# Kernel optimization log

Measured on AMD Instinct MI355X. Metric: run time of the kernel, lower is better.

Reference implementation:

```python
import jax, jax.numpy as jnp
import numpy as np

B, H, OUT, C, O = 4096, 32, 16, 16, 80
N = C + O          # node_num
T = 5              # time_step


def setup_inputs() -> dict:
    key = jax.random.key(0)
    ks = jax.random.split(key, 24)
    x = jax.random.normal(ks[0], (B, N * H), jnp.float32)
    # relation matrix [num_classes, num_objects] -> block adjacency as in load_nodes
    mat = (jax.random.uniform(ks[1], (C, O)) < 0.3).astype(jnp.float32)
    in_mat = jnp.zeros((N, N), jnp.float32).at[:C, C:].set(mat)
    out_mat = jnp.zeros((N, N), jnp.float32).at[C:, :C].set(mat.T)
    mask = (mat > 0).astype(jnp.float32)  # [C, O]

    def W(k, o, i, s=0.1):
        return (jax.random.normal(k, (o, i), jnp.float32) * s)

    return dict(
        input=x, in_mat=in_mat, out_mat=out_mat, mask=mask,
        W3w=W(ks[2], H, 2 * H), b3w=jnp.zeros((H,), jnp.float32),
        W3u=W(ks[3], H, H),     b3u=jnp.zeros((H,), jnp.float32),
        W4w=W(ks[4], H, 2 * H), b4w=jnp.zeros((H,), jnp.float32),
        W5w=W(ks[5], H, 2 * H), b5w=jnp.zeros((H,), jnp.float32),
        W5u=W(ks[6], H, H),     b5u=jnp.zeros((H,), jnp.float32),
        Wo=W(ks[7], OUT, 2 * H), bo=jnp.zeros((OUT,), jnp.float32),
        Wrx=W(ks[8], OUT, H, 0.01), brx=jnp.zeros((OUT,), jnp.float32),
        Wry=W(ks[9], OUT, H, 0.01), bry=jnp.zeros((OUT,), jnp.float32),
        Wr2=W(ks[10], 1, OUT, 0.1), br2=jnp.zeros((1,), jnp.float32),
    )


def reference(input, in_mat, out_mat, mask, W3w, b3w, W3u, b3u, W4w, b4w,
              W5w, b5w, W5u, b5u, Wo, bo, Wrx, brx, Wry, bry, Wr2, br2):
    x0 = input.reshape(B, N, H)
    nodes = x0
    for _ in range(T):
        a_in = jnp.einsum('ij,bjh->bih', in_mat, nodes)
        a_out = jnp.einsum('ij,bjh->bih', out_mat, nodes)
        av = jnp.concatenate([a_in, a_out], axis=-1)          # [B,N,2H]
        u3 = nodes @ W3u.T + b3u
        zv = jax.nn.sigmoid(av @ W3w.T + b3w + u3)
        # NOTE: original code (bug) reuses fc_eq3_u for the reset gate
        rv = jax.nn.sigmoid(av @ W4w.T + b4w + u3)
        hv = jnp.tanh(av @ W5w.T + b5w + (rv * nodes) @ W5u.T + b5u)
        nodes = (1.0 - zv) * nodes + zv * hv
    # per-node output
    out = jnp.tanh(jnp.concatenate([nodes, x0], axis=-1) @ Wo.T + bo)  # [B,N,OUT]
    # pairwise reasoning between class nodes and object nodes
    rfcx = jnp.tanh(nodes[:, :C] @ Wrx.T + brx)   # [B,C,OUT]
    rfcy = jnp.tanh(nodes[:, C:] @ Wry.T + bry)   # [B,O,OUT]
    rocat = rfcx[:, :, None, :] * rfcy[:, None, :, :]              # [B,C,O,OUT]
    rfc2 = jax.nn.sigmoid(rocat @ Wr2.T + br2)                     # [B,C,O,1]
    rfc2 = rfc2 * mask[None, :, :, None]
    routput = out[:, :C]                                           # [B,C,OUT]
    ooutput = out[:, C:]                                           # [B,O,OUT]
    weight_o = ooutput[:, None, :, :] * rfc2                       # [B,C,O,OUT]
    final = jnp.concatenate([routput[:, :, None, :], weight_o], axis=2)  # [B,C,O+1,OUT]
    return final
```

## Files before the change

### kernel.cpp

```cpp
#include <hip/hip_runtime.h>

#define NTH 256

#define S_NDS   0
#define S_AV    3264
#define S_W3U   6528
#define S_W5U   7552
#define S_W3W   8576
#define S_W4W   10624
#define S_W5W   12672
#define S_MASK  14720
#define S_TOT   16016

#define S_WOT   S_W3U
#define S_WRX   S_W5U
#define S_WRY   (S_W5U+512)
#define S_OUTB  S_W3W
#define S_RFCX  S_W4W
#define S_RFCY  (S_W4W+256)
#define S_RFC2  S_AV

__device__ __forceinline__ float sig_(float x) { return 1.0f / (1.0f + __expf(-x)); }
__device__ __forceinline__ float th_(float x)  { return 1.0f - 2.0f / (1.0f + __expf(2.0f * x)); }

union F4 { float4 v; float f[4]; };
union F2 { float2 v; float f[2]; };

__global__ __launch_bounds__(NTH, 2)
void ggnn_fused(const float* __restrict__ input,
                const float* __restrict__ maskp,
                const float* __restrict__ W3w, const float* __restrict__ b3w,
                const float* __restrict__ W3u, const float* __restrict__ b3u,
                const float* __restrict__ W4w, const float* __restrict__ b4w,
                const float* __restrict__ W5w, const float* __restrict__ b5w,
                const float* __restrict__ W5u, const float* __restrict__ b5u,
                const float* __restrict__ Wo,  const float* __restrict__ bo,
                const float* __restrict__ Wrx, const float* __restrict__ brx,
                const float* __restrict__ Wry, const float* __restrict__ bry,
                const float* __restrict__ Wr2, const float* __restrict__ br2,
                float* __restrict__ dout)
{
    __shared__ float S[S_TOT];
    const int tid = threadIdx.x;
    const int b   = blockIdx.x;

    for (int t = tid; t < 1024; t += NTH) {
        const int h = t >> 5, k = t & 31;
        S[S_W3U + k*32 + h] = W3u[t];
        S[S_W5U + k*32 + h] = W5u[t];
    }
    for (int t = tid; t < 2048; t += NTH) {
        const int h = t >> 6, k = t & 63;
        S[S_W3W + k*32 + h] = W3w[t];
        S[S_W4W + k*32 + h] = W4w[t];
        S[S_W5W + k*32 + h] = W5w[t];
    }
    for (int t = tid; t < 1280; t += NTH) {
        const int c = t / 80, o = t - c*80;
        S[S_MASK + c*81 + o] = maskp[t];
    }
    const float* xin = input + (size_t)b * 3072;
    for (int t = tid; t < 3072; t += NTH) {
        const int i = t >> 5, h = t & 31;
        S[S_NDS + i*34 + h] = xin[t];
    }

    const int a  = tid & 31;
    const int bq = tid >> 5;
    const int h0 = bq << 2;
    const int i0 = a, i1 = a + 32, i2 = a + 64;
    const bool isC = (a < 16);

    float bu_[4], bz_[4], br_[4], bh_[4];
    #pragma unroll
    for (int q = 0; q < 4; ++q) {
        bu_[q] = b3u[h0+q];
        bz_[q] = b3w[h0+q];
        br_[q] = b4w[h0+q];
        bh_[q] = b5w[h0+q] + b5u[h0+q];
    }
    __syncthreads();

    for (int it = 0; it < 5; ++it) {
        {
            float a0 = 0.f, a1 = 0.f;
            #pragma unroll 8
            for (int o = 0; o < 80; ++o) {
                const float v = S[S_NDS + (16+o)*34 + a];
                a0 = fmaf(S[S_MASK + bq*81 + o],     v, a0);
                a1 = fmaf(S[S_MASK + (bq+8)*81 + o], v, a1);
            }
            S[S_AV + bq*34 + a]     = a0;
            S[S_AV + (bq+8)*34 + a] = a1;

            float vc[16];
            #pragma unroll
            for (int c = 0; c < 16; ++c) vc[c] = S[S_NDS + c*34 + a];
            #pragma unroll
            for (int tp = 0; tp < 10; ++tp) {
                const int o0 = bq + 8*tp;
                float acc = 0.f;
                #pragma unroll
                for (int c = 0; c < 16; ++c)
                    acc = fmaf(S[S_MASK + c*81 + o0], vc[c], acc);
                S[S_AV + (16+o0)*34 + a] = acc;
            }
        }
        __syncthreads();

        float u0[4],u1[4],u2[4],z0[4],z1[4],z2[4],r0[4],r1[4],r2[4],g0[4],g1[4],g2[4];
        #pragma unroll
        for (int q = 0; q < 4; ++q) {
            u0[q]=bu_[q]; u1[q]=bu_[q]; u2[q]=bu_[q];
            z0[q]=bz_[q]; z1[q]=bz_[q]; z2[q]=bz_[q];
            r0[q]=br_[q]; r1[q]=br_[q]; r2[q]=br_[q];
            g0[q]=bh_[q]; g1[q]=bh_[q]; g2[q]=bh_[q];
        }
        #pragma unroll 2
        for (int k = 0; k < 32; ++k) {
            const float vn0 = S[S_NDS + i0*34 + k];
            const float vn1 = S[S_NDS + i1*34 + k];
            const float vn2 = S[S_NDS + i2*34 + k];
            const float va0 = S[S_AV + i0*34 + k];
            const float va1 = S[S_AV + i1*34 + k];
            const float va2 = S[S_AV + i2*34 + k];
            F4 wu, wzC, wzO, wrC, wrO, whC, whO;
            wu.v  = *(const float4*)&S[S_W3U + k*32 + h0];
            wzC.v = *(const float4*)&S[S_W3W + k*32 + h0];
            wzO.v = *(const float4*)&S[S_W3W + (k+32)*32 + h0];
            wrC.v = *(const float4*)&S[S_W4W + k*32 + h0];
            wrO.v = *(const float4*)&S[S_W4W + (k+32)*32 + h0];
            whC.v = *(const float4*)&S[S_W5W + k*32 + h0];
            whO.v = *(const float4*)&S[S_W5W + (k+32)*32 + h0];
            #pragma unroll
            for (int q = 0; q < 4; ++q) {
                const float wuq = wu.f[q];
                u0[q] = fmaf(wuq, vn0, u0[q]);
                u1[q] = fmaf(wuq, vn1, u1[q]);
                u2[q] = fmaf(wuq, vn2, u2[q]);
                const float wz0 = isC ? wzC.f[q] : wzO.f[q];
                const float wr0 = isC ? wrC.f[q] : wrO.f[q];
                const float wh0 = isC ? whC.f[q] : whO.f[q];
                z0[q] = fmaf(wz0,      va0, z0[q]);
                z1[q] = fmaf(wzO.f[q], va1, z1[q]);
                z2[q] = fmaf(wzO.f[q], va2, z2[q]);
                r0[q] = fmaf(wr0,      va0, r0[q]);
                r1[q] = fmaf(wrO.f[q], va1, r1[q]);
                r2[q] = fmaf(wrO.f[q], va2, r2[q]);
                g0[q] = fmaf(wh0,      va0, g0[q]);
                g1[q] = fmaf(whO.f[q], va1, g1[q]);
                g2[q] = fmaf(whO.f[q], va2, g2[q]);
            }
        }
        float nd0[4], nd1[4], nd2[4];
        #pragma unroll
        for (int q = 0; q < 4; ++q) {
            nd0[q] = S[S_NDS + i0*34 + h0 + q];
            nd1[q] = S[S_NDS + i1*34 + h0 + q];
            nd2[q] = S[S_NDS + i2*34 + h0 + q];
        }
        __syncthreads();
        #pragma unroll
        for (int q = 0; q < 4; ++q) {
            S[S_AV + i0*34 + h0 + q] = sig_(r0[q] + u0[q]) * nd0[q];
            S[S_AV + i1*34 + h0 + q] = sig_(r1[q] + u1[q]) * nd1[q];
            S[S_AV + i2*34 + h0 + q] = sig_(r2[q] + u2[q]) * nd2[q];
        }
        __syncthreads();
        #pragma unroll 4
        for (int k = 0; k < 32; ++k) {
            const float rk0 = S[S_AV + i0*34 + k];
            const float rk1 = S[S_AV + i1*34 + k];
            const float rk2 = S[S_AV + i2*34 + k];
            F4 w5; w5.v = *(const float4*)&S[S_W5U + k*32 + h0];
            #pragma unroll
            for (int q = 0; q < 4; ++q) {
                g0[q] = fmaf(w5.f[q], rk0, g0[q]);
                g1[q] = fmaf(w5.f[q], rk1, g1[q]);
                g2[q] = fmaf(w5.f[q], rk2, g2[q]);
            }
        }
        #pragma unroll
        for (int q = 0; q < 4; ++q) {
            const float zz0 = sig_(z0[q] + u0[q]);
            const float zz1 = sig_(z1[q] + u1[q]);
            const float zz2 = sig_(z2[q] + u2[q]);
            S[S_NDS + i0*34 + h0 + q] = fmaf(zz0, th_(g0[q]) - nd0[q], nd0[q]);
            S[S_NDS + i1*34 + h0 + q] = fmaf(zz1, th_(g1[q]) - nd1[q], nd1[q]);
            S[S_NDS + i2*34 + h0 + q] = fmaf(zz2, th_(g2[q]) - nd2[q], nd2[q]);
        }
        __syncthreads();
    }

    for (int t = tid; t < 3072; t += NTH) {
        const int i = t >> 5, h = t & 31;
        S[S_AV + i*34 + h] = xin[t];
    }
    for (int t = tid; t < 1024; t += NTH) {
        const int j = t >> 6, k = t & 63;
        S[S_WOT + k*16 + j] = Wo[t];
    }
    for (int t = tid; t < 512; t += NTH) {
        const int j = t >> 5, k = t & 31;
        S[S_WRX + k*16 + j] = Wrx[t];
        S[S_WRY + k*16 + j] = Wry[t];
    }
    __syncthreads();

    {
        const int j2 = bq * 2;
        float oa0[2], oa1[2], oa2[2];
        #pragma unroll
        for (int q = 0; q < 2; ++q) { oa0[q] = bo[j2+q]; oa1[q] = bo[j2+q]; oa2[q] = bo[j2+q]; }
        #pragma unroll 2
        for (int k = 0; k < 32; ++k) {
            const float vn0 = S[S_NDS + i0*34 + k];
            const float vn1 = S[S_NDS + i1*34 + k];
            const float vn2 = S[S_NDS + i2*34 + k];
            const float vx0 = S[S_AV + i0*34 + k];
            const float vx1 = S[S_AV + i1*34 + k];
            const float vx2 = S[S_AV + i2*34 + k];
            F2 wn, wx;
            wn.v = *(const float2*)&S[S_WOT + k*16 + j2];
            wx.v = *(const float2*)&S[S_WOT + (32+k)*16 + j2];
            #pragma unroll
            for (int q = 0; q < 2; ++q) {
                oa0[q] = fmaf(wn.f[q], vn0, oa0[q]); oa0[q] = fmaf(wx.f[q], vx0, oa0[q]);
                oa1[q] = fmaf(wn.f[q], vn1, oa1[q]); oa1[q] = fmaf(wx.f[q], vx1, oa1[q]);
                oa2[q] = fmaf(wn.f[q], vn2, oa2[q]); oa2[q] = fmaf(wx.f[q], vx2, oa2[q]);
            }
        }
        #pragma unroll
        for (int q = 0; q < 2; ++q) {
            S[S_OUTB + i0*20 + j2 + q] = th_(oa0[q]);
            S[S_OUTB + i1*20 + j2 + q] = th_(oa1[q]);
            S[S_OUTB + i2*20 + j2 + q] = th_(oa2[q]);
        }
    }
    {
        const int jj = tid & 15, grp = tid >> 4;
        float ax = brx[jj];
        #pragma unroll 4
        for (int k = 0; k < 32; ++k)
            ax = fmaf(S[S_WRX + k*16 + jj], S[S_NDS + grp*34 + k], ax);
        S[S_RFCX + grp*16 + jj] = th_(ax);

        float ay[5];
        #pragma unroll
        for (int t2 = 0; t2 < 5; ++t2) ay[t2] = bry[jj];
        #pragma unroll 2
        for (int k = 0; k < 32; ++k) {
            const float w = S[S_WRY + k*16 + jj];
            #pragma unroll
            for (int t2 = 0; t2 < 5; ++t2)
                ay[t2] = fmaf(w, S[S_NDS + (16 + grp + 16*t2)*34 + k], ay[t2]);
        }
        #pragma unroll
        for (int t2 = 0; t2 < 5; ++t2)
            S[S_RFCY + (grp + 16*t2)*16 + jj] = th_(ay[t2]);
    }
    __syncthreads();

    {
        float wr2r[16];
        #pragma unroll
        for (int j = 0; j < 16; ++j) wr2r[j] = Wr2[j];
        const float br2v = br2[0];
        #pragma unroll
        for (int t2 = 0; t2 < 5; ++t2) {
            const int idx = tid + NTH*t2;
            const int c = idx / 80;
            const int o = idx - c*80;
            float s = br2v;
            #pragma unroll
            for (int j = 0; j < 16; ++j)
                s = fmaf(wr2r[j], S[S_RFCX + c*16 + j] * S[S_RFCY + o*16 + j], s);
            S[S_RFC2 + idx] = sig_(s) * S[S_MASK + c*81 + o];
        }
    }
    __syncthreads();

    {
        float* doutb = dout + (size_t)b * 20736;
        #pragma unroll
        for (int t2 = 0; t2 < 21; ++t2) {
            const int f4 = tid + NTH*t2;
            if (f4 < 5184) {
                const int f   = f4 << 2;
                const int c   = f / 1296;
                const int rem = f - c*1296;
                const int co  = rem >> 4;
                const int k   = rem & 15;
                float4 v;
                if (co == 0) {
                    v = *(const float4*)&S[S_OUTB + c*20 + k];
                } else {
                    const float sc = S[S_RFC2 + c*80 + (co - 1)];
                    const float4 ov = *(const float4*)&S[S_OUTB + (16 + co - 1)*20 + k];
                    v.x = ov.x*sc; v.y = ov.y*sc; v.z = ov.z*sc; v.w = ov.w*sc;
                }
                *(float4*)&doutb[f] = v;
            }
        }
    }
}

extern "C" void kernel_launch(void* const* d_in, const int* in_sizes, int n_in,
                              void* d_out, int out_size, void* d_ws, size_t ws_size,
                              hipStream_t stream) {
    const float* input = (const float*)d_in[0];
    const float* maskp = (const float*)d_in[3];
    const float* W3w = (const float*)d_in[4];  const float* b3w = (const float*)d_in[5];
    const float* W3u = (const float*)d_in[6];  const float* b3u = (const float*)d_in[7];
    const float* W4w = (const float*)d_in[8];  const float* b4w = (const float*)d_in[9];
    const float* W5w = (const float*)d_in[10]; const float* b5w = (const float*)d_in[11];
    const float* W5u = (const float*)d_in[12]; const float* b5u = (const float*)d_in[13];
    const float* Wo  = (const float*)d_in[14]; const float* bo  = (const float*)d_in[15];
    const float* Wrx = (const float*)d_in[16]; const float* brx = (const float*)d_in[17];
    const float* Wry = (const float*)d_in[18]; const float* bry = (const float*)d_in[19];
    const float* Wr2 = (const float*)d_in[20]; const float* br2 = (const float*)d_in[21];

    ggnn_fused<<<dim3(4096), dim3(NTH), 0, stream>>>(
        input, maskp, W3w, b3w, W3u, b3u, W4w, b4w, W5w, b5w, W5u, b5u,
        Wo, bo, Wrx, brx, Wry, bry, Wr2, br2, (float*)d_out);
}
```

Measured before the change: 1.005 ms.

## Move weights to global workspace, shrink LDS, use mask bitmasks and packed FMA

Adds a one-block prep kernel that transposes the weights, folds the biases and packs the adjacency mask into bitmasks in a workspace buffer. The main kernel then reads weights from global memory and cache instead of staging them in LDS. That cuts LDS per block from about 64KB to about 25KB and raises launch bounds to 4 blocks per CU. The adjacency aggregation now uses bitmask selects instead of float mask multiplies, and the GRU matmuls use 2-wide float vectors so the compiler can emit packed FMA. The risk is that weight reads go through the cache instead of LDS, and that register pressure under the tighter launch bound may cause spills.

```diff
diff --git a/kernel.cpp b/kernel.cpp
--- a/kernel.cpp
+++ b/kernel.cpp
@@ -1,264 +1,284 @@
 #include <hip/hip_runtime.h>
 
 #define NTH 256
-
-#define S_NDS   0
-#define S_AV    3264
-#define S_W3U   6528
-#define S_W5U   7552
-#define S_W3W   8576
-#define S_W4W   10624
-#define S_W5W   12672
-#define S_MASK  14720
-#define S_TOT   16016
-
-#define S_WOT   S_W3U
-#define S_WRX   S_W5U
-#define S_WRY   (S_W5U+512)
-#define S_OUTB  S_W3W
-#define S_RFCX  S_W4W
-#define S_RFCY  (S_W4W+256)
-#define S_RFC2  S_AV
+typedef __attribute__((ext_vector_type(2))) float f32x2;
+
+#define WS_WU    0
+#define WS_W5U   1024
+#define WS_WZ    2048
+#define WS_WR    4096
+#define WS_WG    6144
+#define WS_WO    8192
+#define WS_WRX   9216
+#define WS_WRY   9728
+#define WS_BZ    10240
+#define WS_BR    10272
+#define WS_BG    10304
+#define WS_BITC  10336
+#define WS_BITO  10400
+#define WS_TOTAL 10480
 
 __device__ __forceinline__ float sig_(float x) { return 1.0f / (1.0f + __expf(-x)); }
 __device__ __forceinline__ float th_(float x)  { return 1.0f - 2.0f / (1.0f + __expf(2.0f * x)); }
-
-union F4 { float4 v; float f[4]; };
-union F2 { float2 v; float f[2]; };
-
-__global__ __launch_bounds__(NTH, 2)
-void ggnn_fused(const float* __restrict__ input,
-                const float* __restrict__ maskp,
-                const float* __restrict__ W3w, const float* __restrict__ b3w,
-                const float* __restrict__ W3u, const float* __restrict__ b3u,
-                const float* __restrict__ W4w, const float* __restrict__ b4w,
-                const float* __restrict__ W5w, const float* __restrict__ b5w,
-                const float* __restrict__ W5u, const float* __restrict__ b5u,
-                const float* __restrict__ Wo,  const float* __restrict__ bo,
-                const float* __restrict__ Wrx, const float* __restrict__ brx,
-                const float* __restrict__ Wry, const float* __restrict__ bry,
-                const float* __restrict__ Wr2, const float* __restrict__ br2,
-                float* __restrict__ dout)
+__device__ __forceinline__ f32x2 sp(float x) { f32x2 r; r[0] = x; r[1] = x; return r; }
+__device__ __forceinline__ float msel(float v, unsigned bits, int bit) {
+    const int m = (int)(bits << (31 - bit)) >> 31;
+    return __int_as_float(__float_as_int(v) & m);
+}
+
+__global__ void ggnn_prep(const float* __restrict__ mask,
+                          const float* __restrict__ W3w, const float* __restrict__ b3w,
+                          const float* __restrict__ W3u, const float* __restrict__ b3u,
+                          const float* __restrict__ W4w, const float* __restrict__ b4w,
+                          const float* __restrict__ W5w, const float* __restrict__ b5w,
+                          const float* __restrict__ W5u, const float* __restrict__ b5u,
+                          const float* __restrict__ Wo,
+                          const float* __restrict__ Wrx, const float* __restrict__ Wry,
+                          float* __restrict__ ws)
 {
-    __shared__ float S[S_TOT];
+    const int t = threadIdx.x;
+    for (int i = t; i < 1024; i += NTH) {
+        const int k = i >> 5, h = i & 31;
+        ws[WS_WU  + i] = W3u[h*32 + k];
+        ws[WS_W5U + i] = W5u[h*32 + k];
+        ws[WS_WZ + i]        = W3w[h*64 + k];
+        ws[WS_WZ + 1024 + i] = W3w[h*64 + 32 + k];
+        ws[WS_WR + i]        = W4w[h*64 + k];
+        ws[WS_WR + 1024 + i] = W4w[h*64 + 32 + k];
+        ws[WS_WG + i]        = W5w[h*64 + k];
+        ws[WS_WG + 1024 + i] = W5w[h*64 + 32 + k];
+        const int kk = i >> 4, j = i & 15;
+        ws[WS_WO + i] = Wo[j*64 + kk];
+    }
+    for (int i = t; i < 512; i += NTH) {
+        const int k = i >> 4, j = i & 15;
+        ws[WS_WRX + i] = Wrx[j*32 + k];
+        ws[WS_WRY + i] = Wry[j*32 + k];
+    }
+    if (t < 32) {
+        ws[WS_BZ + t] = b3w[t] + b3u[t];
+        ws[WS_BR + t] = b4w[t] + b3u[t];
+        ws[WS_BG + t] = b5w[t] + b5u[t];
+    }
+    unsigned* wsu = (unsigned*)ws;
+    if (t < 64) {
+        const int r = t >> 2, w = t & 3;
+        unsigned bits = 0;
+        for (int bb = 0; bb < 32; ++bb) {
+            const int o = w*32 + bb;
+            if (o < 80 && mask[r*80 + o] > 0.5f) bits |= (1u << bb);
+        }
+        wsu[WS_BITC + t] = bits;
+    }
+    if (t < 80) {
+        unsigned bits = 0;
+        for (int c = 0; c < 16; ++c)
+            if (mask[c*80 + t] > 0.5f) bits |= (1u << c);
+        wsu[WS_BITO + t] = bits;
+    }
+}
+
+__global__ __launch_bounds__(NTH, 4)
+void ggnn_main(const float* __restrict__ input, const float* __restrict__ ws,
+               const float* __restrict__ bo,  const float* __restrict__ brx,
+               const float* __restrict__ bry, const float* __restrict__ Wr2,
+               const float* __restrict__ br2, float* __restrict__ dout)
+{
+    __shared__ float S[6336];
+    float* NOD = S;
+    float* AV  = S + 3168;
     const int tid = threadIdx.x;
     const int b   = blockIdx.x;
-
-    for (int t = tid; t < 1024; t += NTH) {
-        const int h = t >> 5, k = t & 31;
-        S[S_W3U + k*32 + h] = W3u[t];
-        S[S_W5U + k*32 + h] = W5u[t];
-    }
-    for (int t = tid; t < 2048; t += NTH) {
-        const int h = t >> 6, k = t & 63;
-        S[S_W3W + k*32 + h] = W3w[t];
-        S[S_W4W + k*32 + h] = W4w[t];
-        S[S_W5W + k*32 + h] = W5w[t];
-    }
-    for (int t = tid; t < 1280; t += NTH) {
-        const int c = t / 80, o = t - c*80;
-        S[S_MASK + c*81 + o] = maskp[t];
-    }
     const float* xin = input + (size_t)b * 3072;
-    for (int t = tid; t < 3072; t += NTH) {
-        const int i = t >> 5, h = t & 31;
-        S[S_NDS + i*34 + h] = xin[t];
-    }
+    const unsigned* wsu = (const unsigned*)ws;
+
+    for (int t = tid; t < 3072; t += NTH)
+        NOD[(t >> 5)*33 + (t & 31)] = xin[t];
 
     const int a  = tid & 31;
     const int bq = tid >> 5;
     const int h0 = bq << 2;
     const int i0 = a, i1 = a + 32, i2 = a + 64;
-    const bool isC = (a < 16);
-
-    float bu_[4], bz_[4], br_[4], bh_[4];
-    #pragma unroll
-    for (int q = 0; q < 4; ++q) {
-        bu_[q] = b3u[h0+q];
-        bz_[q] = b3w[h0+q];
-        br_[q] = b4w[h0+q];
-        bh_[q] = b5w[h0+q] + b5u[h0+q];
-    }
+    const int sel0 = (a < 16) ? 0 : 1024;
+
+    const float* wuB  = ws + WS_WU + h0;
+    const float* wzB0 = ws + WS_WZ + sel0 + h0;
+    const float* wzBO = ws + WS_WZ + 1024 + h0;
+    const float* wrB0 = ws + WS_WR + sel0 + h0;
+    const float* wrBO = ws + WS_WR + 1024 + h0;
+    const float* wgB0 = ws + WS_WG + sel0 + h0;
+    const float* wgBO = ws + WS_WG + 1024 + h0;
+    const float* w5B  = ws + WS_W5U + h0;
+
     __syncthreads();
 
     for (int it = 0; it < 5; ++it) {
         {
+            unsigned bc0[3], bc1[3];
+            #pragma unroll
+            for (int w = 0; w < 3; ++w) {
+                bc0[w] = wsu[WS_BITC + bq*4 + w];
+                bc1[w] = wsu[WS_BITC + (bq + 8)*4 + w];
+            }
             float a0 = 0.f, a1 = 0.f;
-            #pragma unroll 8
+            #pragma unroll
             for (int o = 0; o < 80; ++o) {
-                const float v = S[S_NDS + (16+o)*34 + a];
-                a0 = fmaf(S[S_MASK + bq*81 + o],     v, a0);
-                a1 = fmaf(S[S_MASK + (bq+8)*81 + o], v, a1);
+                const float v = NOD[(16 + o)*33 + a];
+                a0 += msel(v, bc0[o >> 5], o & 31);
+                a1 += msel(v, bc1[o >> 5], o & 31);
             }
-            S[S_AV + bq*34 + a]     = a0;
-            S[S_AV + (bq+8)*34 + a] = a1;
-
+            AV[bq*33 + a]       = a0;
+            AV[(bq + 8)*33 + a] = a1;
             float vc[16];
             #pragma unroll
-            for (int c = 0; c < 16; ++c) vc[c] = S[S_NDS + c*34 + a];
-            #pragma unroll
-            for (int tp = 0; tp < 10; ++tp) {
-                const int o0 = bq + 8*tp;
+            for (int c = 0; c < 16; ++c) vc[c] = NOD[c*33 + a];
+            #pragma unroll
+            for (int t = 0; t < 10; ++t) {
+                const unsigned bb = wsu[WS_BITO + bq + 8*t];
                 float acc = 0.f;
                 #pragma unroll
-                for (int c = 0; c < 16; ++c)
-                    acc = fmaf(S[S_MASK + c*81 + o0], vc[c], acc);
-                S[S_AV + (16+o0)*34 + a] = acc;
+                for (int c = 0; c < 16; ++c) acc += msel(vc[c], bb, c);
+                AV[(16 + bq + 8*t)*33 + a] = acc;
             }
         }
         __syncthreads();
 
-        float u0[4],u1[4],u2[4],z0[4],z1[4],z2[4],r0[4],r1[4],r2[4],g0[4],g1[4],g2[4];
-        #pragma unroll
-        for (int q = 0; q < 4; ++q) {
-            u0[q]=bu_[q]; u1[q]=bu_[q]; u2[q]=bu_[q];
-            z0[q]=bz_[q]; z1[q]=bz_[q]; z2[q]=bz_[q];
-            r0[q]=br_[q]; r1[q]=br_[q]; r2[q]=br_[q];
-            g0[q]=bh_[q]; g1[q]=bh_[q]; g2[q]=bh_[q];
-        }
+        const f32x2 bzA = *(const f32x2*)(ws + WS_BZ + h0);
+        const f32x2 bzB = *(const f32x2*)(ws + WS_BZ + h0 + 2);
+        const f32x2 brA = *(const f32x2*)(ws + WS_BR + h0);
+        const f32x2 brB = *(const f32x2*)(ws + WS_BR + h0 + 2);
+        const f32x2 bgA = *(const f32x2*)(ws + WS_BG + h0);
+        const f32x2 bgB = *(const f32x2*)(ws + WS_BG + h0 + 2);
+        f32x2 u0A = sp(0.f), u0B = sp(0.f), u1A = sp(0.f), u1B = sp(0.f), u2A = sp(0.f), u2B = sp(0.f);
+        f32x2 z0A = bzA, z0B = bzB, z1A = bzA, z1B = bzB, z2A = bzA, z2B = bzB;
+        f32x2 r0A = brA, r0B = brB, r1A = brA, r1B = brB, r2A = brA, r2B = brB;
+        f32x2 g0A = bgA, g0B = bgB, g1A = bgA, g1B = bgB, g2A = bgA, g2B = bgB;
         #pragma unroll 2
         for (int k = 0; k < 32; ++k) {
-            const float vn0 = S[S_NDS + i0*34 + k];
-            const float vn1 = S[S_NDS + i1*34 + k];
-            const float vn2 = S[S_NDS + i2*34 + k];
-            const float va0 = S[S_AV + i0*34 + k];
-            const float va1 = S[S_AV + i1*34 + k];
-            const float va2 = S[S_AV + i2*34 + k];
-            F4 wu, wzC, wzO, wrC, wrO, whC, whO;
-            wu.v  = *(const float4*)&S[S_W3U + k*32 + h0];
-            wzC.v = *(const float4*)&S[S_W3W + k*32 + h0];
-            wzO.v = *(const float4*)&S[S_W3W + (k+32)*32 + h0];
-            wrC.v = *(const float4*)&S[S_W4W + k*32 + h0];
-            wrO.v = *(const float4*)&S[S_W4W + (k+32)*32 + h0];
-            whC.v = *(const float4*)&S[S_W5W + k*32 + h0];
-            whO.v = *(const float4*)&S[S_W5W + (k+32)*32 + h0];
-            #pragma unroll
-            for (int q = 0; q < 4; ++q) {
-                const float wuq = wu.f[q];
-                u0[q] = fmaf(wuq, vn0, u0[q]);
-                u1[q] = fmaf(wuq, vn1, u1[q]);
-                u2[q] = fmaf(wuq, vn2, u2[q]);
-                const float wz0 = isC ? wzC.f[q] : wzO.f[q];
-                const float wr0 = isC ? wrC.f[q] : wrO.f[q];
-                const float wh0 = isC ? whC.f[q] : whO.f[q];
-                z0[q] = fmaf(wz0,      va0, z0[q]);
-                z1[q] = fmaf(wzO.f[q], va1, z1[q]);
-                z2[q] = fmaf(wzO.f[q], va2, z2[q]);
-                r0[q] = fmaf(wr0,      va0, r0[q]);
-                r1[q] = fmaf(wrO.f[q], va1, r1[q]);
-                r2[q] = fmaf(wrO.f[q], va2, r2[q]);
-                g0[q] = fmaf(wh0,      va0, g0[q]);
-                g1[q] = fmaf(whO.f[q], va1, g1[q]);
-                g2[q] = fmaf(whO.f[q], va2, g2[q]);
-            }
-        }
-        float nd0[4], nd1[4], nd2[4];
+            const int ko = k*32;
+            union { float4 v; f32x2 h[2]; } wu, wz0, wzO, wr0, wrO, wg0, wgO;
+            wu.v  = *(const float4*)(wuB  + ko);
+            wz0.v = *(const float4*)(wzB0 + ko);
+            wzO.v = *(const float4*)(wzBO + ko);
+            wr0.v = *(const float4*)(wrB0 + ko);
+            wrO.v = *(const float4*)(wrBO + ko);
+            wg0.v = *(const float4*)(wgB0 + ko);
+            wgO.v = *(const float4*)(wgBO + ko);
+            const f32x2 n0 = sp(NOD[i0*33 + k]), n1 = sp(NOD[i1*33 + k]), n2 = sp(NOD[i2*33 + k]);
+            const f32x2 v0 = sp(AV[i0*33 + k]),  v1 = sp(AV[i1*33 + k]),  v2 = sp(AV[i2*33 + k]);
+            u0A += wu.h[0]*n0;  u0B += wu.h[1]*n0;
+            u1A += wu.h[0]*n1;  u1B += wu.h[1]*n1;
+            u2A += wu.h[0]*n2;  u2B += wu.h[1]*n2;
+            z0A += wz0.h[0]*v0; z0B += wz0.h[1]*v0;
+            z1A += wzO.h[0]*v1; z1B += wzO.h[1]*v1;
+            z2A += wzO.h[0]*v2; z2B += wzO.h[1]*v2;
+            r0A += wr0.h[0]*v0; r0B += wr0.h[1]*v0;
+            r1A += wrO.h[0]*v1; r1B += wrO.h[1]*v1;
+            r2A += wrO.h[0]*v2; r2B += wrO.h[1]*v2;
+            g0A += wg0.h[0]*v0; g0B += wg0.h[1]*v0;
+            g1A += wgO.h[0]*v1; g1B += wgO.h[1]*v1;
+            g2A += wgO.h[0]*v2; g2B += wgO.h[1]*v2;
+        }
+        float uu0[4] = {u0A[0], u0A[1], u0B[0], u0B[1]};
+        float uu1[4] = {u1A[0], u1A[1], u1B[0], u1B[1]};
+        float uu2[4] = {u2A[0], u2A[1], u2B[0], u2B[1]};
+        float zz0[4] = {z0A[0], z0A[1], z0B[0], z0B[1]};
+        float zz1[4] = {z1A[0], z1A[1], z1B[0], z1B[1]};
+        float zz2[4] = {z2A[0], z2A[1], z2B[0], z2B[1]};
+        float rr0[4] = {r0A[0], r0A[1], r0B[0], r0B[1]};
+        float rr1[4] = {r1A[0], r1A[1], r1B[0], r1B[1]};
+        float rr2[4] = {r2A[0], r2A[1], r2B[0], r2B[1]};
+        float nd0[4], nd1[4], nd2[4], rn0[4], rn1[4], rn2[4];
         #pragma unroll
         for (int q = 0; q < 4; ++q) {
-            nd0[q] = S[S_NDS + i0*34 + h0 + q];
-            nd1[q] = S[S_NDS + i1*34 + h0 + q];
-            nd2[q] = S[S_NDS + i2*34 + h0 + q];
+            nd0[q] = NOD[i0*33 + h0 + q];
+            nd1[q] = NOD[i1*33 + h0 + q];
+            nd2[q] = NOD[i2*33 + h0 + q];
+            zz0[q] = sig_(zz0[q] + uu0[q]);
+            zz1[q] = sig_(zz1[q] + uu1[q]);
+            zz2[q] = sig_(zz2[q] + uu2[q]);
+            rn0[q] = sig_(rr0[q] + uu0[q]) * nd0[q];
+            rn1[q] = sig_(rr1[q] + uu1[q]) * nd1[q];
+            rn2[q] = sig_(rr2[q] + uu2[q]) * nd2[q];
         }
         __syncthreads();
         #pragma unroll
         for (int q = 0; q < 4; ++q) {
-            S[S_AV + i0*34 + h0 + q] = sig_(r0[q] + u0[q]) * nd0[q];
-            S[S_AV + i1*34 + h0 + q] = sig_(r1[q] + u1[q]) * nd1[q];
-            S[S_AV + i2*34 + h0 + q] = sig_(r2[q] + u2[q]) * nd2[q];
+            AV[i0*33 + h0 + q] = rn0[q];
+            AV[i1*33 + h0 + q] = rn1[q];
+            AV[i2*33 + h0 + q] = rn2[q];
         }
         __syncthreads();
-        #pragma unroll 4
-        for (int k = 0; k < 32; ++k) {
-            const float rk0 = S[S_AV + i0*34 + k];
-            const float rk1 = S[S_AV + i1*34 + k];
-            const float rk2 = S[S_AV + i2*34 + k];
-            F4 w5; w5.v = *(const float4*)&S[S_W5U + k*32 + h0];
-            #pragma unroll
-            for (int q = 0; q < 4; ++q) {
-                g0[q] = fmaf(w5.f[q], rk0, g0[q]);
-                g1[q] = fmaf(w5.f[q], rk1, g1[q]);
-                g2[q] = fmaf(w5.f[q], rk2, g2[q]);
-            }
-        }
-        #pragma unroll
-        for (int q = 0; q < 4; ++q) {
-            const float zz0 = sig_(z0[q] + u0[q]);
-            const float zz1 = sig_(z1[q] + u1[q]);
-            const float zz2 = sig_(z2[q] + u2[q]);
-            S[S_NDS + i0*34 + h0 + q] = fmaf(zz0, th_(g0[q]) - nd0[q], nd0[q]);
-            S[S_NDS + i1*34 + h0 + q] = fmaf(zz1, th_(g1[q]) - nd1[q], nd1[q]);
-            S[S_NDS + i2*34 + h0 + q] = fmaf(zz2, th_(g2[q]) - nd2[q], nd2[q]);
-        }
-        __syncthreads();
-    }
-
-    for (int t = tid; t < 3072; t += NTH) {
-        const int i = t >> 5, h = t & 31;
-        S[S_AV + i*34 + h] = xin[t];
-    }
-    for (int t = tid; t < 1024; t += NTH) {
-        const int j = t >> 6, k = t & 63;
-        S[S_WOT + k*16 + j] = Wo[t];
-    }
-    for (int t = tid; t < 512; t += NTH) {
-        const int j = t >> 5, k = t & 31;
-        S[S_WRX + k*16 + j] = Wrx[t];
-        S[S_WRY + k*16 + j] = Wry[t];
-    }
-    __syncthreads();
-
-    {
-        const int j2 = bq * 2;
-        float oa0[2], oa1[2], oa2[2];
-        #pragma unroll
-        for (int q = 0; q < 2; ++q) { oa0[q] = bo[j2+q]; oa1[q] = bo[j2+q]; oa2[q] = bo[j2+q]; }
+
         #pragma unroll 2
         for (int k = 0; k < 32; ++k) {
-            const float vn0 = S[S_NDS + i0*34 + k];
-            const float vn1 = S[S_NDS + i1*34 + k];
-            const float vn2 = S[S_NDS + i2*34 + k];
-            const float vx0 = S[S_AV + i0*34 + k];
-            const float vx1 = S[S_AV + i1*34 + k];
-            const float vx2 = S[S_AV + i2*34 + k];
-            F2 wn, wx;
-            wn.v = *(const float2*)&S[S_WOT + k*16 + j2];
-            wx.v = *(const float2*)&S[S_WOT + (32+k)*16 + j2];
-            #pragma unroll
-            for (int q = 0; q < 2; ++q) {
-                oa0[q] = fmaf(wn.f[q], vn0, oa0[q]); oa0[q] = fmaf(wx.f[q], vx0, oa0[q]);
-                oa1[q] = fmaf(wn.f[q], vn1, oa1[q]); oa1[q] = fmaf(wx.f[q], vx1, oa1[q]);
-                oa2[q] = fmaf(wn.f[q], vn2, oa2[q]); oa2[q] = fmaf(wx.f[q], vx2, oa2[q]);
-            }
-        }
-        #pragma unroll
-        for (int q = 0; q < 2; ++q) {
-            S[S_OUTB + i0*20 + j2 + q] = th_(oa0[q]);
-            S[S_OUTB + i1*20 + j2 + q] = th_(oa1[q]);
-            S[S_OUTB + i2*20 + j2 + q] = th_(oa2[q]);
-        }
-    }
-    {
-        const int jj = tid & 15, grp = tid >> 4;
-        float ax = brx[jj];
-        #pragma unroll 4
-        for (int k = 0; k < 32; ++k)
-            ax = fmaf(S[S_WRX + k*16 + jj], S[S_NDS + grp*34 + k], ax);
-        S[S_RFCX + grp*16 + jj] = th_(ax);
-
-        float ay[5];
-        #pragma unroll
-        for (int t2 = 0; t2 < 5; ++t2) ay[t2] = bry[jj];
-        #pragma unroll 2
-        for (int k = 0; k < 32; ++k) {
-            const float w = S[S_WRY + k*16 + jj];
-            #pragma unroll
-            for (int t2 = 0; t2 < 5; ++t2)
-                ay[t2] = fmaf(w, S[S_NDS + (16 + grp + 16*t2)*34 + k], ay[t2]);
-        }
+            union { float4 v; f32x2 h[2]; } w5;
+            w5.v = *(const float4*)(w5B + k*32);
+            const f32x2 q0 = sp(AV[i0*33 + k]), q1 = sp(AV[i1*33 + k]), q2 = sp(AV[i2*33 + k]);
+            g0A += w5.h[0]*q0; g0B += w5.h[1]*q0;
+            g1A += w5.h[0]*q1; g1B += w5.h[1]*q1;
+            g2A += w5.h[0]*q2; g2B += w5.h[1]*q2;
+        }
+        float gg0[4] = {g0A[0], g0A[1], g0B[0], g0B[1]};
+        float gg1[4] = {g1A[0], g1A[1], g1B[0], g1B[1]};
+        float gg2[4] = {g2A[0], g2A[1], g2B[0], g2B[1]};
+        #pragma unroll
+        for (int q = 0; q < 4; ++q) {
+            NOD[i0*33 + h0 + q] = fmaf(zz0[q], th_(gg0[q]) - nd0[q], nd0[q]);
+            NOD[i1*33 + h0 + q] = fmaf(zz1[q], th_(gg1[q]) - nd1[q], nd1[q]);
+            NOD[i2*33 + h0 + q] = fmaf(zz2[q], th_(gg2[q]) - nd2[q], nd2[q]);
+        }
+        __syncthreads();
+    }
+
+    for (int t = tid; t < 3072; t += NTH)
+        AV[(t >> 5)*33 + (t & 31)] = xin[t];
+    __syncthreads();
+
+    const int j2 = bq * 2;
+    f32x2 oa0 = *(const f32x2*)(bo + j2);
+    f32x2 oa1 = oa0, oa2 = oa0;
+    #pragma unroll 2
+    for (int k = 0; k < 32; ++k) {
+        const f32x2 wn = *(const f32x2*)(ws + WS_WO + k*16 + j2);
+        const f32x2 wx = *(const f32x2*)(ws + WS_WO + (32 + k)*16 + j2);
+        const f32x2 n0 = sp(NOD[i0*33 + k]), n1 = sp(NOD[i1*33 + k]), n2 = sp(NOD[i2*33 + k]);
+        const f32x2 x0 = sp(AV[i0*33 + k]),  x1 = sp(AV[i1*33 + k]),  x2 = sp(AV[i2*33 + k]);
+        oa0 += wn*n0; oa0 += wx*x0;
+        oa1 += wn*n1; oa1 += wx*x1;
+        oa2 += wn*n2; oa2 += wx*x2;
+    }
+    const float ob0[2] = {th_(oa0[0]), th_(oa0[1])};
+    const float ob1[2] = {th_(oa1[0]), th_(oa1[1])};
+    const float ob2[2] = {th_(oa2[0]), th_(oa2[1])};
+
+    const int jj = tid & 15, grp = tid >> 4;
+    float ax = brx[jj];
+    #pragma unroll 4
+    for (int k = 0; k < 32; ++k)
+        ax = fmaf(ws[WS_WRX + k*16 + jj], NOD[grp*33 + k], ax);
+    float ay[5];
+    #pragma unroll
+    for (int t2 = 0; t2 < 5; ++t2) ay[t2] = bry[jj];
+    #pragma unroll 2
+    for (int k = 0; k < 32; ++k) {
+        const float ww = ws[WS_WRY + k*16 + jj];
         #pragma unroll
         for (int t2 = 0; t2 < 5; ++t2)
-            S[S_RFCY + (grp + 16*t2)*16 + jj] = th_(ay[t2]);
-    }
+            ay[t2] = fmaf(ww, NOD[(16 + grp + 16*t2)*33 + k], ay[t2]);
+    }
+    __syncthreads();
+
+    #pragma unroll
+    for (int q = 0; q < 2; ++q) {
+        AV[i0*20 + j2 + q] = ob0[q];
+        AV[i1*20 + j2 + q] = ob1[q];
+        AV[i2*20 + j2 + q] = ob2[q];
+    }
+    NOD[grp*17 + jj] = th_(ax);
+    #pragma unroll
+    for (int t2 = 0; t2 < 5; ++t2)
+        NOD[272 + (grp + 16*t2)*17 + jj] = th_(ay[t2]);
     __syncthreads();
 
     {
@@ -274,8 +294,8 @@
             float s = br2v;
             #pragma unroll
             for (int j = 0; j < 16; ++j)
-                s = fmaf(wr2r[j], S[S_RFCX + c*16 + j] * S[S_RFCY + o*16 + j], s);
-            S[S_RFC2 + idx] = sig_(s) * S[S_MASK + c*81 + o];
+                s = fmaf(wr2r[j], NOD[c*17 + j] * NOD[272 + o*17 + j], s);
+            NOD[1632 + idx] = msel(sig_(s), wsu[WS_BITO + o], c);
         }
     }
     __syncthreads();
@@ -293,10 +313,10 @@
                 const int k   = rem & 15;
                 float4 v;
                 if (co == 0) {
-                    v = *(const float4*)&S[S_OUTB + c*20 + k];
+                    v = *(const float4*)&AV[c*20 + k];
                 } else {
-                    const float sc = S[S_RFC2 + c*80 + (co - 1)];
-                    const float4 ov = *(const float4*)&S[S_OUTB + (16 + co - 1)*20 + k];
+                    const float sc = NOD[1632 + c*80 + (co - 1)];
+                    const float4 ov = *(const float4*)&AV[(16 + co - 1)*20 + k];
                     v.x = ov.x*sc; v.y = ov.y*sc; v.z = ov.z*sc; v.w = ov.w*sc;
                 }
                 *(float4*)&doutb[f] = v;
@@ -319,8 +339,10 @@
     const float* Wrx = (const float*)d_in[16]; const float* brx = (const float*)d_in[17];
     const float* Wry = (const float*)d_in[18]; const float* bry = (const float*)d_in[19];
     const float* Wr2 = (const float*)d_in[20]; const float* br2 = (const float*)d_in[21];
-
-    ggnn_fused<<<dim3(4096), dim3(NTH), 0, stream>>>(
-        input, maskp, W3w, b3w, W3u, b3u, W4w, b4w, W5w, b5w, W5u, b5u,
-        Wo, bo, Wrx, brx, Wry, bry, Wr2, br2, (float*)d_out);
+    float* ws = (float*)d_ws;
+
+    ggnn_prep<<<dim3(1), dim3(NTH), 0, stream>>>(
+        maskp, W3w, b3w, W3u, b3u, W4w, b4w, W5w, b5w, W5u, b5u, Wo, Wrx, Wry, ws);
+    ggnn_main<<<dim3(4096), dim3(NTH), 0, stream>>>(
+        input, ws, bo, brx, bry, Wr2, br2, (float*)d_out);
 }
```

Result: slower. 1.193 ms (+18.7%).
